# Kernel tuning notes

Measured on AMD Instinct MI355X. Metric: run time of the kernel, lower is better.

## Reference

```python
import jax, jax.numpy as jnp
import numpy as np

N_ORDER = 64
PRED_LEN = 720
SEQ_LEN = 720
ENC_IN = 321
BATCH = 16


def _hippo_legs(N):
    # HiPPO-LegS continuous transition (A, B), float64 numpy
    q = np.arange(N, dtype=np.float64)
    col, row = np.meshgrid(q, q)
    r = 2.0 * q + 1.0
    M = -(np.where(row >= col, r, 0.0) - np.diag(q))
    T = np.sqrt(np.diag(2.0 * q + 1.0))
    A = T @ M @ np.linalg.inv(T)
    B = np.diag(T)[:, None].copy()
    return A, B


def _discretize_bilinear(A, B, dt):
    # scipy.signal.cont2discrete(..., method='bilinear') equivalent
    N = A.shape[0]
    I = np.eye(N)
    BL = np.linalg.inv(I - (dt / 2.0) * A)
    Ad = BL @ (I + (dt / 2.0) * A)
    Bd = (BL @ (dt * B)).squeeze(-1)
    return Ad, Bd


def _legendre_eval_matrix(N, dt):
    # ss.eval_legendre(np.arange(N)[:,None], 1 - 2*vals).T via 3-term recurrence
    vals = np.arange(0.0, 1.0, dt)
    x = 1.0 - 2.0 * vals
    Ps = [np.ones_like(x), x]
    for n in range(1, N - 1):
        Ps.append(((2.0 * n + 1.0) * x * Ps[-1] - n * Ps[-2]) / (n + 1.0))
    return np.stack(Ps[:N], axis=0).T  # [len(vals), N]


def setup_inputs() -> dict:
    key = jax.random.key(0)
    k1, k2, k3 = jax.random.split(key, 3)
    dt = 1.0 / PRED_LEN
    A, B = _hippo_legs(N_ORDER)
    Ad, Bd = _discretize_bilinear(A, B, dt)
    eval_matrix = _legendre_eval_matrix(N_ORDER, dt)
    bound = 1.0 / np.sqrt(N_ORDER)  # torch nn.Linear default init range
    return {
        "x_enc": jax.random.normal(k1, (BATCH, SEQ_LEN, ENC_IN), dtype=jnp.float32),
        "A": jnp.asarray(Ad, dtype=jnp.float32),
        "B_vec": jnp.asarray(Bd, dtype=jnp.float32),
        "eval_matrix": jnp.asarray(eval_matrix, dtype=jnp.float32),
        "W_mlp": jax.random.uniform(k2, (N_ORDER, N_ORDER), jnp.float32, -bound, bound),
        "b_mlp": jax.random.uniform(k3, (N_ORDER,), jnp.float32, -bound, bound),
        "affine_weight": jnp.ones((1, 1, ENC_IN), jnp.float32),
        "affine_bias": jnp.zeros((1, 1, ENC_IN), jnp.float32),
    }


def reference(x_enc, A, B_vec, eval_matrix, W_mlp, b_mlp, affine_weight, affine_bias):
    P, N = eval_matrix.shape  # pred_len, proj_degree

    # RevIN-style instance normalization (means/stdev detached in torch)
    means = jax.lax.stop_gradient(jnp.mean(x_enc, axis=1, keepdims=True))
    x = x_enc - means
    stdev = jax.lax.stop_gradient(jnp.sqrt(jnp.var(x, axis=1, keepdims=True) + 1e-5))
    x = x / stdev
    x = x * affine_weight + affine_bias

    x_in = x[:, -P:]                         # [B, P, E]
    xs = jnp.transpose(x_in, (1, 0, 2))      # [P, B, E]: time-major for scan
    c0 = jnp.zeros((x_in.shape[0], x_in.shape[2], N), x_enc.dtype)

    def step(c, f):
        # c_t = c_{t-1} @ A^T + f_t B  (HiPPO-LegS linear recurrence)
        c_new = c @ A.T + f[..., None] * B_vec
        return c_new, c_new

    _, cs = jax.lax.scan(step, c0, xs)       # [P, B, E, N]

    out1 = cs @ W_mlp.T + b_mlp              # mlp over coefficient dim N
    x_dec_c = out1[P - 1]                    # [B, E, N] (seq_len >= pred_len branch)
    x_dec = x_dec_c @ eval_matrix.T          # [B, E, P] Legendre reconstruction
    x_dec = jnp.transpose(x_dec, (0, 2, 1))  # [B, P, E]

    # de-normalize
    x_dec = (x_dec - affine_bias) / (affine_weight + 1e-10)
    x_dec = x_dec * stdev + means
    return x_dec
```

## Files before the change

kernel.cpp:

```cpp
#include <hip/hip_runtime.h>
#include <math.h>

#define BATCH 16
#define SEQ   720
#define ENC   321
#define NORD  64
#define PRED  720
#define NPAIR (BATCH*ENC)

#define WS_KT    0
#define WS_EWT   (WS_KT + PRED*NORD)
#define WS_EVB   (WS_EWT + NORD*PRED)
#define WS_A16   (WS_EVB + PRED)
#define WS_KSUMP (WS_A16 + 4096)
#define WS_G     (WS_KSUMP + 17*64)
#define WS_PSUM  (WS_G + 4*96*4096)
#define WS_PSS   (WS_PSUM + 4*16*6*64)

__global__ __launch_bounds__(256, 1) void prep(const float* __restrict__ A,
        const float* __restrict__ Bv, float* __restrict__ ws)
{
    __shared__ float sv[4][64];
    const int tid  = threadIdx.x;
    const int lane = tid & 63;
    const int wv   = tid >> 6;
    if (blockIdx.x < 16) {
        float ar[64];
        #pragma unroll
        for (int k = 0; k < 16; k++) {
            float4 v = *(const float4*)&A[lane*64 + 4*k];
            ar[4*k]=v.x; ar[4*k+1]=v.y; ar[4*k+2]=v.z; ar[4*k+3]=v.w;
        }
        const int j = blockIdx.x*4 + wv;
        sv[wv][lane] = (lane == j) ? 1.f : 0.f;
        for (int s = 0; s < 16; s++) {
            float acc = 0.f;
            #pragma unroll
            for (int k = 0; k < 16; k++) {
                float4 v = *(const float4*)&sv[wv][4*k];
                acc += ar[4*k]*v.x + ar[4*k+1]*v.y + ar[4*k+2]*v.z + ar[4*k+3]*v.w;
            }
            sv[wv][lane] = acc;
        }
        ws[WS_A16 + lane*64 + j] = sv[wv][lane];
    } else {
        if (tid >= 64) return;
        float ar[64];
        #pragma unroll
        for (int k = 0; k < 16; k++) {
            float4 v = *(const float4*)&A[lane*64 + 4*k];
            ar[4*k]=v.x; ar[4*k+1]=v.y; ar[4*k+2]=v.z; ar[4*k+3]=v.w;
        }
        float* Kt = ws + WS_KT;
        float bv = Bv[lane];
        sv[0][lane] = bv;
        Kt[(size_t)719*64 + lane] = bv;
        float ksml = bv;
        for (int j = 1; j <= 15; j++) {
            float acc = 0.f;
            #pragma unroll
            for (int k = 0; k < 16; k++) {
                float4 v = *(const float4*)&sv[0][4*k];
                acc += ar[4*k]*v.x + ar[4*k+1]*v.y + ar[4*k+2]*v.z + ar[4*k+3]*v.w;
            }
            sv[0][lane] = acc;
            Kt[(size_t)(719 - j)*64 + lane] = acc;
            ksml += acc;
        }
        ws[WS_KSUMP + 16*64 + lane] = ksml;
    }
}

__global__ __launch_bounds__(256, 1) void chainsEW(const float* __restrict__ evalm,
        const float* __restrict__ W, const float* __restrict__ bm,
        float* __restrict__ ws)
{
    __shared__ float dsm[8224];
    const int tid  = threadIdx.x;
    const int lane = tid & 63;
    const int wv   = tid >> 6;
    if (blockIdx.x < 16) {
        if (tid >= 64) return;
        float* sv = dsm;
        const int r = blockIdx.x;
        const float* A16 = ws + WS_A16;
        float* Kt = ws + WS_KT;
        float ar16[64];
        #pragma unroll
        for (int k = 0; k < 16; k++) {
            float4 v = *(const float4*)&A16[lane*64 + 4*k];
            ar16[4*k]=v.x; ar16[4*k+1]=v.y; ar16[4*k+2]=v.z; ar16[4*k+3]=v.w;
        }
        float ksml = 0.f;
        sv[lane] = Kt[(size_t)(719 - r)*64 + lane];
        for (int j = r + 16; j <= 719; j += 16) {
            float acc = 0.f;
            #pragma unroll
            for (int k = 0; k < 16; k++) {
                float4 v = *(const float4*)&sv[4*k];
                acc += ar16[4*k]*v.x + ar16[4*k+1]*v.y + ar16[4*k+2]*v.z + ar16[4*k+3]*v.w;
            }
            sv[lane] = acc;
            Kt[(size_t)(719 - j)*64 + lane] = acc;
            ksml += acc;
        }
        ws[WS_KSUMP + r*64 + lane] = ksml;
    } else {
        float* smW = dsm;
        float* Et  = dsm + 4160;
        const int r = blockIdx.x - 16;
        for (int idx = tid; idx < 4096; idx += 256)
            smW[(idx>>6)*65 + (idx&63)] = W[idx];
        __syncthreads();
        float bv = bm[lane];
        #pragma unroll
        for (int k = 0; k < 15; k++) {
            int row = wv + k*4;
            int tp = r*60 + row;
            const float* ev = evalm + (size_t)tp*64;
            float acc = 0.f;
            #pragma unroll
            for (int kk = 0; kk < 16; kk++) {
                float4 e4 = *(const float4*)&ev[4*kk];
                acc += e4.x*smW[(4*kk+0)*65+lane] + e4.y*smW[(4*kk+1)*65+lane]
                     + e4.z*smW[(4*kk+2)*65+lane] + e4.w*smW[(4*kk+3)*65+lane];
            }
            Et[lane*61 + row] = acc;
            float pv = ev[lane] * bv;
            #pragma unroll
            for (int o = 32; o > 0; o >>= 1) pv += __shfl_down(pv, o);
            if (lane == 0) ws[WS_EVB + tp] = pv;
        }
        __syncthreads();
        for (int idx = tid; idx < 4096; idx += 256) {
            int m = idx >> 6, row = idx & 63;
            if (row < 60)
                ws[WS_EWT + (size_t)m*720 + r*60 + row] = Et[m*61 + row];
        }
    }
}

__device__ inline float4 ldx(const float* __restrict__ x, int b, int t, int e4)
{
    float4 r = make_float4(0.f,0.f,0.f,0.f);
    const float* p = x + ((size_t)b*SEQ + t)*ENC;
    if (e4 + 3 < ENC) r = *(const float4*)&p[e4];
    else {
        if (e4   < ENC) r.x = p[e4];
        if (e4+1 < ENC) r.y = p[e4+1];
        if (e4+2 < ENC) r.z = p[e4+2];
    }
    return r;
}

__global__ __launch_bounds__(256) void k2(const float* __restrict__ x,
        float* __restrict__ ws)
{
    __shared__ float xt[2][12*64];
    __shared__ float ks[2][12*64];
    __shared__ float redn[12*64];
    __shared__ float reds[12*64];
    const int tid = threadIdx.x;
    const int bid = blockIdx.x;
    const int b = bid / 24, rem = bid % 24;
    const int et = rem / 4, tsp = rem % 4;
    const int e0 = et*64, t0 = tsp*180;

    const bool xon = tid < 192;
    const bool kon = tid >= 64;
    const int sx_t  = tid >> 4;
    const int sx_e4 = (tid & 15) * 4;
    const int sk    = tid - 64;
    const int sk_t  = sk >> 4;
    const int sk_m4 = (sk & 15) * 4;

    const float* Kt = ws + WS_KT;
    float s0=0,s1=0,s2=0,s3=0, q0=0,q1=0,q2=0,q3=0;
    float4 rx = make_float4(0,0,0,0), rk = make_float4(0,0,0,0);

    if (xon) rx = ldx(x, b, t0 + sx_t, e0 + sx_e4);
    if (kon) rk = *(const float4*)&Kt[(size_t)(t0 + sk_t)*64 + sk_m4];
    if (xon) {
        *(float4*)&xt[0][sx_t*64 + sx_e4] = rx;
        s0+=rx.x; s1+=rx.y; s2+=rx.z; s3+=rx.w;
        q0+=rx.x*rx.x; q1+=rx.y*rx.y; q2+=rx.z*rx.z; q3+=rx.w*rx.w;
    }
    if (kon) *(float4*)&ks[0][sk_t*64 + sk_m4] = rk;

    const int lane = tid & 63, wv = tid >> 6;
    const int elg = lane & 15;
    const int mgr = wv*4 + (lane >> 4);
    float acc[4][4];
    #pragma unroll
    for (int j = 0; j < 4; j++)
        #pragma unroll
        for (int i = 0; i < 4; i++) acc[j][i] = 0.f;

    for (int ch = 0; ch < 15; ch++) {
        if (ch + 1 < 15) {
            if (xon) rx = ldx(x, b, t0 + (ch+1)*12 + sx_t, e0 + sx_e4);
            if (kon) rk = *(const float4*)&Kt[(size_t)(t0 + (ch+1)*12 + sk_t)*64 + sk_m4];
        }
        __syncthreads();
        const float* xb = xt[ch & 1];
        const float* kb = ks[ch & 1];
        #pragma unroll
        for (int tt = 0; tt < 12; tt++) {
            float4 f  = *(const float4*)&xb[tt*64 + elg*4];
            float4 kv = *(const float4*)&kb[tt*64 + mgr*4];
            acc[0][0]+=f.x*kv.x; acc[0][1]+=f.x*kv.y; acc[0][2]+=f.x*kv.z; acc[0][3]+=f.x*kv.w;
            acc[1][0]+=f.y*kv.x; acc[1][1]+=f.y*kv.y; acc[1][2]+=f.y*kv.z; acc[1][3]+=f.y*kv.w;
            acc[2][0]+=f.z*kv.x; acc[2][1]+=f.z*kv.y; acc[2][2]+=f.z*kv.z; acc[2][3]+=f.z*kv.w;
            acc[3][0]+=f.w*kv.x; acc[3][1]+=f.w*kv.y; acc[3][2]+=f.w*kv.z; acc[3][3]+=f.w*kv.w;
        }
        if (ch + 1 < 15) {
            if (xon) {
                *(float4*)&xt[(ch+1)&1][sx_t*64 + sx_e4] = rx;
                s0+=rx.x; s1+=rx.y; s2+=rx.z; s3+=rx.w;
                q0+=rx.x*rx.x; q1+=rx.y*rx.y; q2+=rx.z*rx.z; q3+=rx.w*rx.w;
            }
            if (kon) *(float4*)&ks[(ch+1)&1][sk_t*64 + sk_m4] = rk;
        }
    }

    float* g = ws + WS_G + (size_t)(tsp*96 + b*6 + et)*4096;
    #pragma unroll
    for (int i = 0; i < 4; i++)
        *(float4*)&g[(mgr*4 + i)*64 + elg*4] =
            make_float4(acc[0][i], acc[1][i], acc[2][i], acc[3][i]);

    __syncthreads();
    if (xon) {
        redn[sx_t*64 + sx_e4+0] = s0; redn[sx_t*64 + sx_e4+1] = s1;
        redn[sx_t*64 + sx_e4+2] = s2; redn[sx_t*64 + sx_e4+3] = s3;
        reds[sx_t*64 + sx_e4+0] = q0; reds[sx_t*64 + sx_e4+1] = q1;
        reds[sx_t*64 + sx_e4+2] = q2; reds[sx_t*64 + sx_e4+3] = q3;
    }
    __syncthreads();
    if (tid < 64) {
        float s = 0.f, q = 0.f;
        #pragma unroll
        for (int rr = 0; rr < 12; rr++) { s += redn[rr*64 + tid]; q += reds[rr*64 + tid]; }
        const size_t o = (size_t)((tsp*16 + b)*6 + et)*64 + tid;
        ws[WS_PSUM + o] = s;
        ws[WS_PSS  + o] = q;
    }
}

__global__ __launch_bounds__(256) void k3f(const float* __restrict__ aw,
        const float* __restrict__ ab, const float* __restrict__ ws,
        float* __restrict__ out)
{
    __shared__ float Cm[64*132];
    __shared__ float EWm[64*68];
    __shared__ float ssc[128], ssh[128], smean[128], ssd[128], siaw[128], sabe[128];
    __shared__ float kss[64];
    const int tid = threadIdx.x;
    const int b   = blockIdx.x / 12;
    const int rr  = blockIdx.x % 12;
    const int eT  = rr / 4;
    const int tq  = rr % 4;
    const int e0  = eT * 128;
    const int et0 = eT * 2;

    if (tid < 128) {
        const int el = tid, e = e0 + el;
        const int et = et0 + (el >> 6), eli = el & 63;
        float s = 0.f, q = 0.f;
        #pragma unroll
        for (int tsp = 0; tsp < 4; tsp++) {
            const size_t o = (size_t)((tsp*16 + b)*6 + et)*64 + eli;
            s += ws[WS_PSUM + o];
            q += ws[WS_PSS  + o];
        }
        float mean = s * (1.0f/SEQ);
        float var  = q * (1.0f/SEQ) - mean*mean;
        float sd   = sqrtf(var + 1e-5f);
        if (e < ENC) {
            float a = aw[e], av = ab[e];
            float sc = a / sd;
            ssc[el] = sc; ssh[el] = av - mean*sc;
            smean[el] = mean; ssd[el] = sd;
            siaw[el] = 1.0f/(a + 1e-10f); sabe[el] = av;
        } else {
            ssc[el]=0.f; ssh[el]=0.f; smean[el]=0.f; ssd[el]=0.f; siaw[el]=0.f; sabe[el]=0.f;
        }
    }
    if (tid < 64) {
        float s = 0.f;
        #pragma unroll
        for (int p = 0; p < 17; p++) s += ws[WS_KSUMP + p*64 + tid];
        kss[tid] = s;
    }
    __syncthreads();

    const float* G = ws + WS_G;
    #pragma unroll
    for (int k = 0; k < 8; k++) {
        int slot = k*256 + tid;
        int m = slot >> 5, el4 = (slot & 31) * 4;
        int et = et0 + (el4 >> 6), eli4 = el4 & 63;
        size_t base = (size_t)(b*6 + et)*4096 + m*64 + eli4;
        float4 g0 = *(const float4*)&G[base];
        float4 g1 = *(const float4*)&G[base + (size_t) 96*4096];
        float4 g2 = *(const float4*)&G[base + (size_t)192*4096];
        float4 g3 = *(const float4*)&G[base + (size_t)288*4096];
        float km = kss[m];
        float4 c;
        c.x = ssc[el4+0]*(g0.x+g1.x+g2.x+g3.x) + ssh[el4+0]*km;
        c.y = ssc[el4+1]*(g0.y+g1.y+g2.y+g3.y) + ssh[el4+1]*km;
        c.z = ssc[el4+2]*(g0.z+g1.z+g2.z+g3.z) + ssh[el4+2]*km;
        c.w = ssc[el4+3]*(g0.w+g1.w+g2.w+g3.w) + ssh[el4+3]*km;
        *(float4*)&Cm[m*132 + el4] = c;
    }
    __syncthreads();

    const float* EWT = ws + WS_EWT;
    const float* evb = ws + WS_EVB;
    const int tx = tid & 31;
    const int ty = tid >> 5;
    for (int ti = 0; ti < 3; ti++) {
        const int tt0 = (tq*3 + ti) * 64;
        if (ti > 0) __syncthreads();
        #pragma unroll
        for (int k = 0; k < 4; k++) {
            int slot = k*256 + tid;
            int m = slot >> 4, t4 = (slot & 15)*4;
            int tp = tt0 + t4;
            float4 v;
            if (tp + 3 < PRED) v = *(const float4*)&EWT[(size_t)m*720 + tp];
            else {
                v = make_float4(0.f,0.f,0.f,0.f);
                if (tp   < PRED) v.x = EWT[(size_t)m*720 + tp];
                if (tp+1 < PRED) v.y = EWT[(size_t)m*720 + tp+1];
                if (tp+2 < PRED) v.z = EWT[(size_t)m*720 + tp+2];
            }
            *(float4*)&EWm[m*68 + t4] = v;
        }
        __syncthreads();

        float acc[8][4];
        #pragma unroll
        for (int i = 0; i < 8; i++)
            #pragma unroll
            for (int j = 0; j < 4; j++) acc[i][j] = 0.f;

        #pragma unroll 4
        for (int m = 0; m < 64; m++) {
            float4 c4 = *(const float4*)&Cm[m*132 + tx*4];
            float4 w0 = *(const float4*)&EWm[m*68 + ty*8];
            float4 w1 = *(const float4*)&EWm[m*68 + ty*8 + 4];
            acc[0][0]+=w0.x*c4.x; acc[0][1]+=w0.x*c4.y; acc[0][2]+=w0.x*c4.z; acc[0][3]+=w0.x*c4.w;
            acc[1][0]+=w0.y*c4.x; acc[1][1]+=w0.y*c4.y; acc[1][2]+=w0.y*c4.z; acc[1][3]+=w0.y*c4.w;
            acc[2][0]+=w0.z*c4.x; acc[2][1]+=w0.z*c4.y; acc[2][2]+=w0.z*c4.z; acc[2][3]+=w0.z*c4.w;
            acc[3][0]+=w0.w*c4.x; acc[3][1]+=w0.w*c4.y; acc[3][2]+=w0.w*c4.z; acc[3][3]+=w0.w*c4.w;
            acc[4][0]+=w1.x*c4.x; acc[4][1]+=w1.x*c4.y; acc[4][2]+=w1.x*c4.z; acc[4][3]+=w1.x*c4.w;
            acc[5][0]+=w1.y*c4.x; acc[5][1]+=w1.y*c4.y; acc[5][2]+=w1.y*c4.z; acc[5][3]+=w1.y*c4.w;
            acc[6][0]+=w1.z*c4.x; acc[6][1]+=w1.z*c4.y; acc[6][2]+=w1.z*c4.z; acc[6][3]+=w1.z*c4.w;
            acc[7][0]+=w1.w*c4.x; acc[7][1]+=w1.w*c4.y; acc[7][2]+=w1.w*c4.z; acc[7][3]+=w1.w*c4.w;
        }

        const int elb = tx*4;
        const int ebase = e0 + elb;
        #pragma unroll
        for (int i = 0; i < 8; i++) {
            int tp = tt0 + ty*8 + i;
            if (tp < PRED) {
                float ev = evb[tp];
                float* op = out + ((size_t)b*PRED + tp)*ENC;
                #pragma unroll
                for (int j = 0; j < 4; j++) {
                    int e = ebase + j;
                    if (e < ENC)
                        op[e] = (acc[i][j] + ev - sabe[elb+j]) * siaw[elb+j] * ssd[elb+j]
                                + smean[elb+j];
                }
            }
        }
    }
}

extern "C" void kernel_launch(void* const* d_in, const int* in_sizes, int n_in,
                              void* d_out, int out_size, void* d_ws, size_t ws_size,
                              hipStream_t stream)
{
    const float* x     = (const float*)d_in[0];
    const float* A     = (const float*)d_in[1];
    const float* Bv    = (const float*)d_in[2];
    const float* evalm = (const float*)d_in[3];
    const float* W     = (const float*)d_in[4];
    const float* bm    = (const float*)d_in[5];
    const float* aw    = (const float*)d_in[6];
    const float* ab    = (const float*)d_in[7];
    float* ws  = (float*)d_ws;
    float* out = (float*)d_out;

    prep    <<<17, 256, 0, stream>>>(A, Bv, ws);
    chainsEW<<<28, 256, 0, stream>>>(evalm, W, bm, ws);
    k2      <<<BATCH*6*4, 256, 0, stream>>>(x, ws);
    k3f     <<<192, 256, 0, stream>>>(aw, ab, ws, out);
}
```

Baseline: 159.1 us.

## Split matvec accumulators, register-cache W, retile gram kernel, vectorize epilogue

```diff
diff --git a/kernel.cpp b/kernel.cpp
--- a/kernel.cpp
+++ b/kernel.cpp
@@ -17,6 +17,26 @@
 #define WS_PSUM  (WS_G + 4*96*4096)
 #define WS_PSS   (WS_PSUM + 4*16*6*64)
 
+#define MV4(AR, SVP, OUTV) do {                                                   \
+    float _a0=0.f,_a1=0.f,_a2=0.f,_a3=0.f;                                        \
+    _Pragma("unroll")                                                             \
+    for (int _k = 0; _k < 4; _k++) {                                              \
+        float4 _v0 = *(const float4*)&(SVP)[16*_k];                               \
+        float4 _v1 = *(const float4*)&(SVP)[16*_k+4];                             \
+        float4 _v2 = *(const float4*)&(SVP)[16*_k+8];                             \
+        float4 _v3 = *(const float4*)&(SVP)[16*_k+12];                            \
+        _a0 += (AR)[16*_k+0]*_v0.x + (AR)[16*_k+1]*_v0.y                          \
+             + (AR)[16*_k+2]*_v0.z + (AR)[16*_k+3]*_v0.w;                         \
+        _a1 += (AR)[16*_k+4]*_v1.x + (AR)[16*_k+5]*_v1.y                          \
+             + (AR)[16*_k+6]*_v1.z + (AR)[16*_k+7]*_v1.w;                         \
+        _a2 += (AR)[16*_k+8]*_v2.x + (AR)[16*_k+9]*_v2.y                          \
+             + (AR)[16*_k+10]*_v2.z + (AR)[16*_k+11]*_v2.w;                       \
+        _a3 += (AR)[16*_k+12]*_v3.x + (AR)[16*_k+13]*_v3.y                        \
+             + (AR)[16*_k+14]*_v3.z + (AR)[16*_k+15]*_v3.w;                       \
+    }                                                                             \
+    OUTV = (_a0+_a1)+(_a2+_a3);                                                   \
+} while (0)
+
 __global__ __launch_bounds__(256, 1) void prep(const float* __restrict__ A,
         const float* __restrict__ Bv, float* __restrict__ ws)
 {
@@ -34,13 +54,9 @@
         const int j = blockIdx.x*4 + wv;
         sv[wv][lane] = (lane == j) ? 1.f : 0.f;
         for (int s = 0; s < 16; s++) {
-            float acc = 0.f;
-            #pragma unroll
-            for (int k = 0; k < 16; k++) {
-                float4 v = *(const float4*)&sv[wv][4*k];
-                acc += ar[4*k]*v.x + ar[4*k+1]*v.y + ar[4*k+2]*v.z + ar[4*k+3]*v.w;
-            }
-            sv[wv][lane] = acc;
+            float nv;
+            MV4(ar, &sv[wv][0], nv);
+            sv[wv][lane] = nv;
         }
         ws[WS_A16 + lane*64 + j] = sv[wv][lane];
     } else {
@@ -57,15 +73,11 @@
         Kt[(size_t)719*64 + lane] = bv;
         float ksml = bv;
         for (int j = 1; j <= 15; j++) {
-            float acc = 0.f;
-            #pragma unroll
-            for (int k = 0; k < 16; k++) {
-                float4 v = *(const float4*)&sv[0][4*k];
-                acc += ar[4*k]*v.x + ar[4*k+1]*v.y + ar[4*k+2]*v.z + ar[4*k+3]*v.w;
-            }
-            sv[0][lane] = acc;
-            Kt[(size_t)(719 - j)*64 + lane] = acc;
-            ksml += acc;
+            float nv;
+            MV4(ar, &sv[0][0], nv);
+            sv[0][lane] = nv;
+            Kt[(size_t)(719 - j)*64 + lane] = nv;
+            ksml += nv;
         }
         ws[WS_KSUMP + 16*64 + lane] = ksml;
     }
@@ -75,7 +87,7 @@
         const float* __restrict__ W, const float* __restrict__ bm,
         float* __restrict__ ws)
 {
-    __shared__ float dsm[8224];
+    __shared__ float dsm[64*61];
     const int tid  = threadIdx.x;
     const int lane = tid & 63;
     const int wv   = tid >> 6;
@@ -94,38 +106,42 @@
         float ksml = 0.f;
         sv[lane] = Kt[(size_t)(719 - r)*64 + lane];
         for (int j = r + 16; j <= 719; j += 16) {
-            float acc = 0.f;
-            #pragma unroll
-            for (int k = 0; k < 16; k++) {
-                float4 v = *(const float4*)&sv[4*k];
-                acc += ar16[4*k]*v.x + ar16[4*k+1]*v.y + ar16[4*k+2]*v.z + ar16[4*k+3]*v.w;
-            }
-            sv[lane] = acc;
-            Kt[(size_t)(719 - j)*64 + lane] = acc;
-            ksml += acc;
+            float nv;
+            MV4(ar16, sv, nv);
+            sv[lane] = nv;
+            Kt[(size_t)(719 - j)*64 + lane] = nv;
+            ksml += nv;
         }
         ws[WS_KSUMP + r*64 + lane] = ksml;
     } else {
-        float* smW = dsm;
-        float* Et  = dsm + 4160;
+        float* Et = dsm;
         const int r = blockIdx.x - 16;
-        for (int idx = tid; idx < 4096; idx += 256)
-            smW[(idx>>6)*65 + (idx&63)] = W[idx];
-        __syncthreads();
+        float wcol[64];
+        #pragma unroll
+        for (int n = 0; n < 64; n++) wcol[n] = W[n*64 + lane];
         float bv = bm[lane];
         #pragma unroll
         for (int k = 0; k < 15; k++) {
             int row = wv + k*4;
             int tp = r*60 + row;
             const float* ev = evalm + (size_t)tp*64;
-            float acc = 0.f;
+            float a0=0.f,a1=0.f,a2=0.f,a3=0.f;
             #pragma unroll
-            for (int kk = 0; kk < 16; kk++) {
-                float4 e4 = *(const float4*)&ev[4*kk];
-                acc += e4.x*smW[(4*kk+0)*65+lane] + e4.y*smW[(4*kk+1)*65+lane]
-                     + e4.z*smW[(4*kk+2)*65+lane] + e4.w*smW[(4*kk+3)*65+lane];
+            for (int kk = 0; kk < 4; kk++) {
+                float4 e0_ = *(const float4*)&ev[16*kk];
+                float4 e1_ = *(const float4*)&ev[16*kk+4];
+                float4 e2_ = *(const float4*)&ev[16*kk+8];
+                float4 e3_ = *(const float4*)&ev[16*kk+12];
+                a0 += e0_.x*wcol[16*kk+0] + e0_.y*wcol[16*kk+1]
+                    + e0_.z*wcol[16*kk+2] + e0_.w*wcol[16*kk+3];
+                a1 += e1_.x*wcol[16*kk+4] + e1_.y*wcol[16*kk+5]
+                    + e1_.z*wcol[16*kk+6] + e1_.w*wcol[16*kk+7];
+                a2 += e2_.x*wcol[16*kk+8] + e2_.y*wcol[16*kk+9]
+                    + e2_.z*wcol[16*kk+10] + e2_.w*wcol[16*kk+11];
+                a3 += e3_.x*wcol[16*kk+12] + e3_.y*wcol[16*kk+13]
+                    + e3_.z*wcol[16*kk+14] + e3_.w*wcol[16*kk+15];
             }
-            Et[lane*61 + row] = acc;
+            Et[lane*61 + row] = (a0+a1)+(a2+a3);
             float pv = ev[lane] * bv;
             #pragma unroll
             for (int o = 32; o > 0; o >>= 1) pv += __shfl_down(pv, o);
@@ -187,12 +203,12 @@
     }
     if (kon) *(float4*)&ks[0][sk_t*64 + sk_m4] = rk;
 
-    const int lane = tid & 63, wv = tid >> 6;
-    const int elg = lane & 15;
-    const int mgr = wv*4 + (lane >> 4);
-    float acc[4][4];
+    const bool con = tid < 128;
+    const int elg = tid & 7;
+    const int mgr = tid >> 3;
+    float acc[8][4];
     #pragma unroll
-    for (int j = 0; j < 4; j++)
+    for (int j = 0; j < 8; j++)
         #pragma unroll
         for (int i = 0; i < 4; i++) acc[j][i] = 0.f;
 
@@ -204,14 +220,21 @@
         __syncthreads();
         const float* xb = xt[ch & 1];
         const float* kb = ks[ch & 1];
-        #pragma unroll
-        for (int tt = 0; tt < 12; tt++) {
-            float4 f  = *(const float4*)&xb[tt*64 + elg*4];
-            float4 kv = *(const float4*)&kb[tt*64 + mgr*4];
-            acc[0][0]+=f.x*kv.x; acc[0][1]+=f.x*kv.y; acc[0][2]+=f.x*kv.z; acc[0][3]+=f.x*kv.w;
-            acc[1][0]+=f.y*kv.x; acc[1][1]+=f.y*kv.y; acc[1][2]+=f.y*kv.z; acc[1][3]+=f.y*kv.w;
-            acc[2][0]+=f.z*kv.x; acc[2][1]+=f.z*kv.y; acc[2][2]+=f.z*kv.z; acc[2][3]+=f.z*kv.w;
-            acc[3][0]+=f.w*kv.x; acc[3][1]+=f.w*kv.y; acc[3][2]+=f.w*kv.z; acc[3][3]+=f.w*kv.w;
+        if (con) {
+            #pragma unroll
+            for (int tt = 0; tt < 12; tt++) {
+                float4 fa = *(const float4*)&xb[tt*64 + elg*8];
+                float4 fb = *(const float4*)&xb[tt*64 + elg*8 + 4];
+                float4 kv = *(const float4*)&kb[tt*64 + mgr*4];
+                acc[0][0]+=fa.x*kv.x; acc[0][1]+=fa.x*kv.y; acc[0][2]+=fa.x*kv.z; acc[0][3]+=fa.x*kv.w;
+                acc[1][0]+=fa.y*kv.x; acc[1][1]+=fa.y*kv.y; acc[1][2]+=fa.y*kv.z; acc[1][3]+=fa.y*kv.w;
+                acc[2][0]+=fa.z*kv.x; acc[2][1]+=fa.z*kv.y; acc[2][2]+=fa.z*kv.z; acc[2][3]+=fa.z*kv.w;
+                acc[3][0]+=fa.w*kv.x; acc[3][1]+=fa.w*kv.y; acc[3][2]+=fa.w*kv.z; acc[3][3]+=fa.w*kv.w;
+                acc[4][0]+=fb.x*kv.x; acc[4][1]+=fb.x*kv.y; acc[4][2]+=fb.x*kv.z; acc[4][3]+=fb.x*kv.w;
+                acc[5][0]+=fb.y*kv.x; acc[5][1]+=fb.y*kv.y; acc[5][2]+=fb.y*kv.z; acc[5][3]+=fb.y*kv.w;
+                acc[6][0]+=fb.z*kv.x; acc[6][1]+=fb.z*kv.y; acc[6][2]+=fb.z*kv.z; acc[6][3]+=fb.z*kv.w;
+                acc[7][0]+=fb.w*kv.x; acc[7][1]+=fb.w*kv.y; acc[7][2]+=fb.w*kv.z; acc[7][3]+=fb.w*kv.w;
+            }
         }
         if (ch + 1 < 15) {
             if (xon) {
@@ -223,11 +246,15 @@
         }
     }
 
-    float* g = ws + WS_G + (size_t)(tsp*96 + b*6 + et)*4096;
-    #pragma unroll
-    for (int i = 0; i < 4; i++)
-        *(float4*)&g[(mgr*4 + i)*64 + elg*4] =
-            make_float4(acc[0][i], acc[1][i], acc[2][i], acc[3][i]);
+    if (con) {
+        float* g = ws + WS_G + (size_t)(tsp*96 + b*6 + et)*4096;
+        #pragma unroll
+        for (int i = 0; i < 4; i++) {
+            float* gr = g + (mgr*4 + i)*64 + elg*8;
+            *(float4*)&gr[0] = make_float4(acc[0][i], acc[1][i], acc[2][i], acc[3][i]);
+            *(float4*)&gr[4] = make_float4(acc[4][i], acc[5][i], acc[6][i], acc[7][i]);
+        }
+    }
 
     __syncthreads();
     if (xon) {
@@ -306,11 +333,13 @@
         float4 g2 = *(const float4*)&G[base + (size_t)192*4096];
         float4 g3 = *(const float4*)&G[base + (size_t)288*4096];
         float km = kss[m];
+        float4 sc = *(const float4*)&ssc[el4];
+        float4 sh = *(const float4*)&ssh[el4];
         float4 c;
-        c.x = ssc[el4+0]*(g0.x+g1.x+g2.x+g3.x) + ssh[el4+0]*km;
-        c.y = ssc[el4+1]*(g0.y+g1.y+g2.y+g3.y) + ssh[el4+1]*km;
-        c.z = ssc[el4+2]*(g0.z+g1.z+g2.z+g3.z) + ssh[el4+2]*km;
-        c.w = ssc[el4+3]*(g0.w+g1.w+g2.w+g3.w) + ssh[el4+3]*km;
+        c.x = sc.x*(g0.x+g1.x+g2.x+g3.x) + sh.x*km;
+        c.y = sc.y*(g0.y+g1.y+g2.y+g3.y) + sh.y*km;
+        c.z = sc.z*(g0.z+g1.z+g2.z+g3.z) + sh.z*km;
+        c.w = sc.w*(g0.w+g1.w+g2.w+g3.w) + sh.w*km;
         *(float4*)&Cm[m*132 + el4] = c;
     }
     __syncthreads();
@@ -319,6 +348,14 @@
     const float* evb = ws + WS_EVB;
     const int tx = tid & 31;
     const int ty = tid >> 5;
+
+    const int elb = tx*4;
+    const int ebase = e0 + elb;
+    float4 sab  = *(const float4*)&sabe[elb];
+    float4 sia  = *(const float4*)&siaw[elb];
+    float4 ssd4 = *(const float4*)&ssd[elb];
+    float4 smn  = *(const float4*)&smean[elb];
+
     for (int ti = 0; ti < 3; ti++) {
         const int tt0 = (tq*3 + ti) * 64;
         if (ti > 0) __syncthreads();
@@ -360,20 +397,23 @@
             acc[7][0]+=w1.w*c4.x; acc[7][1]+=w1.w*c4.y; acc[7][2]+=w1.w*c4.z; acc[7][3]+=w1.w*c4.w;
         }
 
-        const int elb = tx*4;
-        const int ebase = e0 + elb;
         #pragma unroll
         for (int i = 0; i < 8; i++) {
             int tp = tt0 + ty*8 + i;
             if (tp < PRED) {
                 float ev = evb[tp];
                 float* op = out + ((size_t)b*PRED + tp)*ENC;
-                #pragma unroll
-                for (int j = 0; j < 4; j++) {
-                    int e = ebase + j;
-                    if (e < ENC)
-                        op[e] = (acc[i][j] + ev - sabe[elb+j]) * siaw[elb+j] * ssd[elb+j]
-                                + smean[elb+j];
+                if (ebase + 3 < ENC) {
+                    float4 o;
+                    o.x = (acc[i][0] + ev - sab.x) * sia.x * ssd4.x + smn.x;
+                    o.y = (acc[i][1] + ev - sab.y) * sia.y * ssd4.y + smn.y;
+                    o.z = (acc[i][2] + ev - sab.z) * sia.z * ssd4.z + smn.z;
+                    o.w = (acc[i][3] + ev - sab.w) * sia.w * ssd4.w + smn.w;
+                    *(float4*)&op[ebase] = o;
+                } else {
+                    if (ebase   < ENC) op[ebase  ] = (acc[i][0]+ev-sab.x)*sia.x*ssd4.x+smn.x;
+                    if (ebase+1 < ENC) op[ebase+1] = (acc[i][1]+ev-sab.y)*sia.y*ssd4.y+smn.y;
+                    if (ebase+2 < ENC) op[ebase+2] = (acc[i][2]+ev-sab.z)*sia.z*ssd4.z+smn.z;
                 }
             }
         }
```

New measurement: 151.4 us. 4.8% less time.
